# Kernel tuning notes

Measured on AMD Instinct MI355X. Metric: run time of the kernel, lower is better.

## Reference

```python
import jax, jax.numpy as jnp
import numpy as np

S = 128           # seq_len
B = 256           # input_bits (bits per token, also neurons per head)
H = 16            # num_heads
NB = 12           # n_bits_per_neuron -> LUT size 2^12
PB = 7            # relative-position bits = ceil(log2(max_seq_len))
HEAD_IN = 2 * B + PB   # concat(query, key, rel_pos_bits) = 519
THRESH = H // 2


def setup_inputs() -> dict:
    key = jax.random.key(0)
    k1, k2, k3 = jax.random.split(key, 3)
    tokens = jax.random.randint(k1, (S, B), 0, 2, dtype=jnp.int32)           # binary token bits
    memory = jax.random.normal(k2, (H, B, 2 ** NB), dtype=jnp.float32)       # RAM LUT contents per head/neuron
    connections = jax.random.randint(k3, (H, B, NB), 0, HEAD_IN, dtype=jnp.int32)  # per-neuron input-bit wiring
    return {"tokens": tokens, "memory": memory, "connections": connections}


def reference(tokens, memory, connections):
    idx = jnp.arange(S)
    rel = idx[:, None] - idx[None, :]                         # [S,S] i - j
    mask = (rel >= 0).astype(jnp.int32)                        # causal mask (j <= i)
    relc = jnp.clip(rel, 0, S - 1)
    # relative-distance binary encoding, LSB first: [S,S,PB]
    pos_bits = ((relc[..., None] >> jnp.arange(PB)) & 1).astype(jnp.int32)
    q = jnp.broadcast_to(tokens[:, None, :], (S, S, B))
    k = jnp.broadcast_to(tokens[None, :, :], (S, S, B))
    head_in = jnp.concatenate([q, k, pos_bits], axis=-1)       # [S,S,HEAD_IN]
    # RAM address per (query i, key j, head h, neuron n): pack NB wired bits, LSB first
    addr = jnp.zeros((S, S, H, B), dtype=jnp.int32)
    for b in range(NB):  # tiny fixed loop over bit planes, fully vectorized over S,S,H,B
        addr = addr + (head_in[..., connections[:, :, b]] << b)
    # LUT gather: memory[h, n, addr] -> [S,S,H,B]
    h_idx = jnp.arange(H)[:, None]
    n_idx = jnp.arange(B)[None, :]
    vals = memory[h_idx, n_idx, addr]
    bits = (vals > 0.0).astype(jnp.int32)                      # RAM neuron output bit
    # XOR accumulation over attended keys == masked sum mod 2: [S,H,B]
    head_res = jnp.sum(bits * mask[:, :, None, None], axis=1) % 2
    # majority vote across heads per bit
    ones_count = jnp.sum(head_res, axis=1)                     # [S,B]
    return (ones_count > THRESH).astype(jnp.int32)
```

## Files before the change

kernel.cpp:

```cpp
#include <hip/hip_runtime.h>
#include <hip/hip_bf16.h>


#define S 128
#define B 256
#define H 16
#define NB 12

__device__ __forceinline__ unsigned sig(unsigned x) {
    return x ^ ((x >> 3) & 0x70u) ^ ((x >> 6) & 0x70u);
}

__global__ __launch_bounds__(1024) void softram_kernel(
    const int* __restrict__ tokens,
    const float* __restrict__ memory,
    const int* __restrict__ connections,
    int* __restrict__ out)
{
    const int n    = blockIdx.x;
    const int tid  = threadIdx.x;
    const int h    = tid >> 6;
    const int lane = tid & 63;

    __shared__ unsigned char  bytetab[H * 4096];
    __shared__ unsigned int   tokT[8][S];
    __shared__ unsigned short aqsig[H][S];
    __shared__ unsigned short aksig[H][S];
    __shared__ unsigned short apsig[H][S];
    __shared__ int            conns[H][NB];
    __shared__ unsigned int   parts[H][4];

    {
        int i = tid >> 3, w = tid & 7;
        const int4* tp = (const int4*)tokens;
        unsigned v = 0;
        #pragma unroll
        for (int u = 0; u < 8; ++u) {
            int4 x = tp[i * 64 + w * 8 + u];
            v |= (unsigned)(x.x & 1) << (4 * u + 0);
            v |= (unsigned)(x.y & 1) << (4 * u + 1);
            v |= (unsigned)(x.z & 1) << (4 * u + 2);
            v |= (unsigned)(x.w & 1) << (4 * u + 3);
        }
        tokT[w][i] = v;
    }
    if (tid < H * NB) {
        int hh = tid / NB, b = tid - hh * NB;
        conns[hh][b] = connections[hh * (B * NB) + n * NB + b];
    }
    __syncthreads();

    const float4* mrow = (const float4*)(memory + ((size_t)(h * 256 + n) << 12));
    float4 va[16];
    #pragma unroll
    for (int t = 0; t < 16; ++t) va[t] = mrow[lane + 64 * t];

    unsigned qmask = 0, kmask = 0, pmask = 0;
    #pragma unroll
    for (int b = 0; b < NB; ++b) {
        int c = conns[h][b];
        qmask |= (unsigned)(c < 256) << b;
        kmask |= (unsigned)(c >= 256 && c < 512) << b;
        pmask |= (unsigned)(c >= 512) << b;
    }

    #pragma unroll
    for (int e = 0; e < 2; ++e) {
        int ii = lane + 64 * e;
        unsigned aq = 0, ak = 0, ap = 0;
        #pragma unroll
        for (int b = 0; b < NB; ++b) {
            int c = conns[h][b];
            if (c < 256) {
                aq |= ((tokT[c >> 5][ii] >> (c & 31)) & 1u) << b;
            } else if (c < 512) {
                int c2 = c - 256;
                ak |= ((tokT[c2 >> 5][ii] >> (c2 & 31)) & 1u) << b;
            } else {
                ap |= ((unsigned)(ii >> (c - 512)) & 1u) << b;
            }
        }
        aqsig[h][ii] = (unsigned short)sig(aq);
        aksig[h][ii] = (unsigned short)sig(ak);
        apsig[h][ii] = (unsigned short)sig(ap);
    }

    unsigned char* __restrict__ bt = &bytetab[h << 12];
    #pragma unroll
    for (int t = 0; t < 16; ++t) {
        float4 v = va[t];
        unsigned p = 4u * (unsigned)(lane + 64 * t);
        unsigned w = (unsigned)(v.x > 0.f)
                   | ((unsigned)(v.y > 0.f) << 8)
                   | ((unsigned)(v.z > 0.f) << 16)
                   | ((unsigned)(v.w > 0.f) << 24);
        *(unsigned*)&bt[sig(p)] = w;
    }

    unsigned long long rlo = 0, rhi = 0;

    if (pmask == 0) {
        int qb = __popc(qmask), kb = __popc(kmask);
        bool sideQ = (qb <= kb);
        unsigned smask = sideQ ? qmask : kmask;
        int m = sideQ ? qb : kb;
        unsigned spread = 0;
        {
            unsigned k = (unsigned)lane;
            #pragma unroll
            for (int b = 0; b < NB; ++b) {
                if ((smask >> b) & 1u) { spread |= (k & 1u) << b; k >>= 1; }
            }
        }
        const unsigned spv = sig(spread);
        const int lim = 1 << m;
        const bool lv = (lane < lim);
        const unsigned long long vmask =
            (lim >= 64) ? ~0ull : ((1ull << lim) - 1ull);

        if (sideQ) {
            unsigned acc = 0;
            for (int s8 = 0; s8 < 16; ++s8) {
                uint4 uq = *(const uint4*)&aqsig[h][s8 * 8];
                uint4 uk = *(const uint4*)&aksig[h][s8 * 8];
                #pragma unroll
                for (int t = 0; t < 8; ++t) {
                    int j = s8 * 8 + t;
                    unsigned cwk = ((const unsigned*)&uk)[t >> 1];
                    unsigned cwq = ((const unsigned*)&uq)[t >> 1];
                    unsigned akv = (cwk >> ((t & 1) * 16)) & 0xffffu;
                    unsigned aqv = (cwq >> ((t & 1) * 16)) & 0xffffu;
                    acc ^= bt[akv ^ spv];
                    unsigned long long accB = __ballot((acc & 1u) != 0u);
                    unsigned long long mm   = __ballot(lv && (spv == aqv));
                    unsigned long long bit  = ((accB & mm & vmask) != 0ull);
                    if (j < 64) rlo |= bit << j; else rhi |= bit << (j - 64);
                }
            }
        } else {
            unsigned c = 0;
            for (int s8 = 0; s8 < 16; ++s8) {
                uint4 uq = *(const uint4*)&aqsig[h][s8 * 8];
                uint4 uk = *(const uint4*)&aksig[h][s8 * 8];
                #pragma unroll
                for (int t = 0; t < 8; ++t) {
                    int i = s8 * 8 + t;
                    unsigned cwk = ((const unsigned*)&uk)[t >> 1];
                    unsigned cwq = ((const unsigned*)&uq)[t >> 1];
                    unsigned akv = (cwk >> ((t & 1) * 16)) & 0xffffu;
                    unsigned aqv = (cwq >> ((t & 1) * 16)) & 0xffffu;
                    c ^= (unsigned)(lv && (spv == akv));
                    unsigned sb = bt[aqv ^ spv];
                    unsigned long long mb = __ballot((c & sb & 1u) != 0u);
                    unsigned long long bit = (unsigned long long)
                        (__popcll(mb & vmask) & 1ull);
                    if (i < 64) rlo |= bit << i; else rhi |= bit << (i - 64);
                }
            }
        }
    } else {
        const unsigned ak0 = aksig[h][lane];
        const unsigned ak1 = aksig[h][lane + 64];
        for (int s8 = 0; s8 < 16; ++s8) {
            uint4 uq = *(const uint4*)&aqsig[h][s8 * 8];
            #pragma unroll
            for (int t = 0; t < 8; ++t) {
                int i = s8 * 8 + t;
                unsigned cwq = ((const unsigned*)&uq)[t >> 1];
                unsigned aqv = (cwq >> ((t & 1) * 16)) & 0xffffu;
                unsigned ap0 = apsig[h][(i - lane) & 127];
                unsigned v0  = bt[aqv ^ ak0 ^ ap0];
                unsigned long long m0 = __ballot((v0 & 1u) != 0u);
                unsigned long long pre0 =
                    (i >= 63) ? ~0ull : ((2ull << i) - 1ull);
                unsigned cnt = (unsigned)__popcll(m0 & pre0);
                if (i >= 64) {
                    unsigned ap1 = apsig[h][(i - lane - 64) & 127];
                    unsigned v1  = bt[aqv ^ ak1 ^ ap1];
                    unsigned long long m1 = __ballot((v1 & 1u) != 0u);
                    unsigned long long pre1 =
                        (i >= 127) ? ~0ull : ((2ull << (i - 64)) - 1ull);
                    cnt += (unsigned)__popcll(m1 & pre1);
                }
                unsigned long long bit = cnt & 1u;
                if (i < 64) rlo |= bit << i; else rhi |= bit << (i - 64);
            }
        }
    }

    if (lane == 0) {
        parts[h][0] = (unsigned)rlo;
        parts[h][1] = (unsigned)(rlo >> 32);
        parts[h][2] = (unsigned)rhi;
        parts[h][3] = (unsigned)(rhi >> 32);
    }
    __syncthreads();

    if (tid < S) {
        int i = tid, tot = 0;
        #pragma unroll
        for (int hh = 0; hh < H; ++hh)
            tot += (parts[hh][i >> 5] >> (i & 31)) & 1;
        out[i * B + n] = (tot > (H / 2)) ? 1 : 0;
    }
}

extern "C" void kernel_launch(void* const* d_in, const int* in_sizes, int n_in,
                              void* d_out, int out_size, void* d_ws, size_t ws_size,
                              hipStream_t stream) {
    const int*   tokens      = (const int*)d_in[0];
    const float* memory      = (const float*)d_in[1];
    const int*   connections = (const int*)d_in[2];
    int*         out         = (int*)d_out;
    (void)in_sizes; (void)n_in; (void)out_size; (void)d_ws; (void)ws_size;

    softram_kernel<<<B, 1024, 0, stream>>>(tokens, memory, connections, out);
}
```

Baseline: 112.3 us.

## Restructure no-position path into lane-indexed LUT bitmask with scalar key prefix XOR

```diff
diff --git a/kernel.cpp b/kernel.cpp
--- a/kernel.cpp
+++ b/kernel.cpp
@@ -1,5 +1,4 @@
 #include <hip/hip_runtime.h>
-#include <hip/hip_bf16.h>
 
 
 #define S 128
@@ -11,7 +10,7 @@
     return x ^ ((x >> 3) & 0x70u) ^ ((x >> 6) & 0x70u);
 }
 
-__global__ __launch_bounds__(1024) void softram_kernel(
+__global__ __launch_bounds__(1024, 4) void softram_kernel(
     const int* __restrict__ tokens,
     const float* __restrict__ memory,
     const int* __restrict__ connections,
@@ -24,11 +23,15 @@
 
     __shared__ unsigned char  bytetab[H * 4096];
     __shared__ unsigned int   tokT[8][S];
-    __shared__ unsigned short aqsig[H][S];
-    __shared__ unsigned short aksig[H][S];
-    __shared__ unsigned short apsig[H][S];
+    __shared__ unsigned short akT[H][S];
+    __shared__ unsigned short apt[H][S];
     __shared__ int            conns[H][NB];
     __shared__ unsigned int   parts[H][4];
+
+    const float4* mrow = (const float4*)(memory + ((size_t)(h * 256 + n) << 12));
+    float4 va[16];
+    #pragma unroll
+    for (int t = 0; t < 16; ++t) va[t] = mrow[lane + 64 * t];
 
     {
         int i = tid >> 3, w = tid & 7;
@@ -49,11 +52,6 @@
         conns[hh][b] = connections[hh * (B * NB) + n * NB + b];
     }
     __syncthreads();
-
-    const float4* mrow = (const float4*)(memory + ((size_t)(h * 256 + n) << 12));
-    float4 va[16];
-    #pragma unroll
-    for (int t = 0; t < 16; ++t) va[t] = mrow[lane + 64 * t];
 
     unsigned qmask = 0, kmask = 0, pmask = 0;
     #pragma unroll
@@ -63,129 +61,214 @@
         kmask |= (unsigned)(c >= 256 && c < 512) << b;
         pmask |= (unsigned)(c >= 512) << b;
     }
-
-    #pragma unroll
-    for (int e = 0; e < 2; ++e) {
-        int ii = lane + 64 * e;
-        unsigned aq = 0, ak = 0, ap = 0;
-        #pragma unroll
-        for (int b = 0; b < NB; ++b) {
-            int c = conns[h][b];
-            if (c < 256) {
-                aq |= ((tokT[c >> 5][ii] >> (c & 31)) & 1u) << b;
-            } else if (c < 512) {
-                int c2 = c - 256;
-                ak |= ((tokT[c2 >> 5][ii] >> (c2 & 31)) & 1u) << b;
-            } else {
-                ap |= ((unsigned)(ii >> (c - 512)) & 1u) << b;
-            }
-        }
-        aqsig[h][ii] = (unsigned short)sig(aq);
-        aksig[h][ii] = (unsigned short)sig(ak);
-        apsig[h][ii] = (unsigned short)sig(ap);
-    }
+    const int qb = __popc(qmask);
+    const int kb = __popc(kmask);
 
     unsigned char* __restrict__ bt = &bytetab[h << 12];
-    #pragma unroll
-    for (int t = 0; t < 16; ++t) {
-        float4 v = va[t];
-        unsigned p = 4u * (unsigned)(lane + 64 * t);
-        unsigned w = (unsigned)(v.x > 0.f)
-                   | ((unsigned)(v.y > 0.f) << 8)
-                   | ((unsigned)(v.z > 0.f) << 16)
-                   | ((unsigned)(v.w > 0.f) << 24);
-        *(unsigned*)&bt[sig(p)] = w;
-    }
-
     unsigned long long rlo = 0, rhi = 0;
 
     if (pmask == 0) {
-        int qb = __popc(qmask), kb = __popc(kmask);
-        bool sideQ = (qb <= kb);
-        unsigned smask = sideQ ? qmask : kmask;
-        int m = sideQ ? qb : kb;
-        unsigned spread = 0;
+        unsigned qcls0 = 0, qcls1 = 0;
+        #pragma unroll
+        for (int e = 0; e < 2; ++e) {
+            int ii = lane + 64 * e;
+            unsigned qc = 0, kc = 0;
+            int qn = 0, kn = 0;
+            #pragma unroll
+            for (int b = 0; b < NB; ++b) {
+                int c = conns[h][b];
+                if (c < 256) {
+                    qc |= ((tokT[c >> 5][ii] >> (c & 31)) & 1u) << qn;
+                    ++qn;
+                } else {
+                    int c2 = c - 256;
+                    kc |= ((tokT[c2 >> 5][ii] >> (c2 & 31)) & 1u) << kn;
+                    ++kn;
+                }
+            }
+            akT[h][ii] = (unsigned short)kc;
+            if (e == 0) qcls0 = qc; else qcls1 = qc;
+        }
+
+        #pragma unroll
+        for (int t = 0; t < 16; ++t) {
+            float4 v = va[t];
+            unsigned p = 4u * (unsigned)(lane + 64 * t);
+            unsigned w = (unsigned)(v.x > 0.f)
+                       | ((unsigned)(v.y > 0.f) << 8)
+                       | ((unsigned)(v.z > 0.f) << 16)
+                       | ((unsigned)(v.w > 0.f) << 24);
+            *(unsigned*)&bt[sig(p)] = w;
+        }
+
+        const bool formA = (qb <= 6);
+        const int SBITS  = formA ? qb : kb;
+        unsigned apl = 0, aul = 0;
         {
-            unsigned k = (unsigned)lane;
+            int scnt = 0, lcnt = 0;
             #pragma unroll
             for (int b = 0; b < NB; ++b) {
-                if ((smask >> b) & 1u) { spread |= (k & 1u) << b; k >>= 1; }
-            }
-        }
-        const unsigned spv = sig(spread);
-        const int lim = 1 << m;
-        const bool lv = (lane < lim);
-        const unsigned long long vmask =
-            (lim >= 64) ? ~0ull : ((1ull << lim) - 1ull);
-
-        if (sideQ) {
-            unsigned acc = 0;
-            for (int s8 = 0; s8 < 16; ++s8) {
-                uint4 uq = *(const uint4*)&aqsig[h][s8 * 8];
-                uint4 uk = *(const uint4*)&aksig[h][s8 * 8];
+                int c = conns[h][b];
+                bool isS = formA ? (c < 256) : (c >= 256);
+                if (isS) {
+                    apl |= (((unsigned)lane >> scnt) & 1u) << b;
+                    ++scnt;
+                } else {
+                    int p = SBITS + lcnt;
+                    if (p < 6) apl |= (((unsigned)lane >> p) & 1u) << b;
+                    else       aul |= (((unsigned)lane >> (p - 6)) & 1u) << b;
+                    ++lcnt;
+                }
+            }
+        }
+        const unsigned spl  = sig(apl);
+        const unsigned saul = sig(aul);
+        unsigned Wlo = 0, Whi = 0;
+        #pragma unroll 8
+        for (int it = 0; it < 64; ++it) {
+            unsigned sau  = (unsigned)__builtin_amdgcn_readlane((int)saul, it);
+            unsigned bitv = bt[sau ^ spl] & 1u;
+            unsigned long long Bm = __ballot(bitv != 0u);
+            Wlo = (lane == it) ? (unsigned)Bm : Wlo;
+            Whi = (lane == it) ? (unsigned)(Bm >> 32) : Whi;
+        }
+
+        if (formA) {
+            unsigned long long A = 0, cap0 = 0, cap1 = 0;
+            for (int s8 = 0; s8 < 8; ++s8) {
+                uint4 uk = *(const uint4*)&akT[h][s8 * 8];
                 #pragma unroll
                 for (int t = 0; t < 8; ++t) {
                     int j = s8 * 8 + t;
-                    unsigned cwk = ((const unsigned*)&uk)[t >> 1];
-                    unsigned cwq = ((const unsigned*)&uq)[t >> 1];
-                    unsigned akv = (cwk >> ((t & 1) * 16)) & 0xffffu;
-                    unsigned aqv = (cwq >> ((t & 1) * 16)) & 0xffffu;
-                    acc ^= bt[akv ^ spv];
-                    unsigned long long accB = __ballot((acc & 1u) != 0u);
-                    unsigned long long mm   = __ballot(lv && (spv == aqv));
-                    unsigned long long bit  = ((accB & mm & vmask) != 0ull);
-                    if (j < 64) rlo |= bit << j; else rhi |= bit << (j - 64);
-                }
-            }
-        } else {
-            unsigned c = 0;
-            for (int s8 = 0; s8 < 16; ++s8) {
-                uint4 uq = *(const uint4*)&aqsig[h][s8 * 8];
-                uint4 uk = *(const uint4*)&aksig[h][s8 * 8];
+                    unsigned w = ((const unsigned*)&uk)[t >> 1];
+                    unsigned widx = (unsigned)__builtin_amdgcn_readfirstlane(
+                        (int)((w >> ((t & 1) * 16)) & 0xffffu));
+                    unsigned g0 = widx << qb;
+                    int lsel = (int)(g0 >> 6);
+                    unsigned lo = (unsigned)__builtin_amdgcn_readlane((int)Wlo, lsel);
+                    unsigned hi = (unsigned)__builtin_amdgcn_readlane((int)Whi, lsel);
+                    A ^= ((((unsigned long long)hi << 32) | lo) >> (g0 & 63u));
+                    cap0 = (lane == j) ? A : cap0;
+                }
+            }
+            for (int s8 = 8; s8 < 16; ++s8) {
+                uint4 uk = *(const uint4*)&akT[h][s8 * 8];
                 #pragma unroll
                 for (int t = 0; t < 8; ++t) {
-                    int i = s8 * 8 + t;
-                    unsigned cwk = ((const unsigned*)&uk)[t >> 1];
-                    unsigned cwq = ((const unsigned*)&uq)[t >> 1];
-                    unsigned akv = (cwk >> ((t & 1) * 16)) & 0xffffu;
-                    unsigned aqv = (cwq >> ((t & 1) * 16)) & 0xffffu;
-                    c ^= (unsigned)(lv && (spv == akv));
-                    unsigned sb = bt[aqv ^ spv];
-                    unsigned long long mb = __ballot((c & sb & 1u) != 0u);
-                    unsigned long long bit = (unsigned long long)
-                        (__popcll(mb & vmask) & 1ull);
-                    if (i < 64) rlo |= bit << i; else rhi |= bit << (i - 64);
-                }
-            }
+                    int j = s8 * 8 + t;
+                    unsigned w = ((const unsigned*)&uk)[t >> 1];
+                    unsigned widx = (unsigned)__builtin_amdgcn_readfirstlane(
+                        (int)((w >> ((t & 1) * 16)) & 0xffffu));
+                    unsigned g0 = widx << qb;
+                    int lsel = (int)(g0 >> 6);
+                    unsigned lo = (unsigned)__builtin_amdgcn_readlane((int)Wlo, lsel);
+                    unsigned hi = (unsigned)__builtin_amdgcn_readlane((int)Whi, lsel);
+                    A ^= ((((unsigned long long)hi << 32) | lo) >> (g0 & 63u));
+                    cap1 = (lane == j - 64) ? A : cap1;
+                }
+            }
+            rlo = __ballot(((cap0 >> qcls0) & 1ull) != 0ull);
+            rhi = __ballot(((cap1 >> qcls1) & 1ull) != 0ull);
+        } else {
+            unsigned Cw = 0, cap0 = 0, cap1 = 0;
+            for (int s8 = 0; s8 < 8; ++s8) {
+                uint4 uk = *(const uint4*)&akT[h][s8 * 8];
+                #pragma unroll
+                for (int t = 0; t < 8; ++t) {
+                    int j = s8 * 8 + t;
+                    unsigned w = ((const unsigned*)&uk)[t >> 1];
+                    unsigned widx = (unsigned)__builtin_amdgcn_readfirstlane(
+                        (int)((w >> ((t & 1) * 16)) & 0xffffu));
+                    Cw ^= 1u << widx;
+                    cap0 = (lane == j) ? Cw : cap0;
+                }
+            }
+            for (int s8 = 8; s8 < 16; ++s8) {
+                uint4 uk = *(const uint4*)&akT[h][s8 * 8];
+                #pragma unroll
+                for (int t = 0; t < 8; ++t) {
+                    int j = s8 * 8 + t;
+                    unsigned w = ((const unsigned*)&uk)[t >> 1];
+                    unsigned widx = (unsigned)__builtin_amdgcn_readfirstlane(
+                        (int)((w >> ((t & 1) * 16)) & 0xffffu));
+                    Cw ^= 1u << widx;
+                    cap1 = (lane == j - 64) ? Cw : cap1;
+                }
+            }
+            unsigned g0a = qcls0 << kb, g0b = qcls1 << kb;
+            unsigned lo0 = (unsigned)__shfl((int)Wlo, (int)(g0a >> 6));
+            unsigned hi0 = (unsigned)__shfl((int)Whi, (int)(g0a >> 6));
+            unsigned lo1 = (unsigned)__shfl((int)Wlo, (int)(g0b >> 6));
+            unsigned hi1 = (unsigned)__shfl((int)Whi, (int)(g0b >> 6));
+            unsigned W0 = (unsigned)((((unsigned long long)hi0 << 32) | lo0) >> (g0a & 63u));
+            unsigned W1 = (unsigned)((((unsigned long long)hi1 << 32) | lo1) >> (g0b & 63u));
+            rlo = __ballot((__popc(W0 & cap0) & 1) != 0);
+            rhi = __ballot((__popc(W1 & cap1) & 1) != 0);
         }
     } else {
-        const unsigned ak0 = aksig[h][lane];
-        const unsigned ak1 = aksig[h][lane + 64];
-        for (int s8 = 0; s8 < 16; ++s8) {
-            uint4 uq = *(const uint4*)&aqsig[h][s8 * 8];
+        unsigned aqv0 = 0, aqv1 = 0;
+        #pragma unroll
+        for (int e = 0; e < 2; ++e) {
+            int ii = lane + 64 * e;
+            unsigned aq = 0, ak = 0, ap = 0;
+            #pragma unroll
+            for (int b = 0; b < NB; ++b) {
+                int c = conns[h][b];
+                if (c < 256) {
+                    aq |= ((tokT[c >> 5][ii] >> (c & 31)) & 1u) << b;
+                } else if (c < 512) {
+                    int c2 = c - 256;
+                    ak |= ((tokT[c2 >> 5][ii] >> (c2 & 31)) & 1u) << b;
+                } else {
+                    ap |= (((unsigned)ii >> (c - 512)) & 1u) << b;
+                }
+            }
+            akT[h][ii] = (unsigned short)sig(ak);
+            apt[h][ii] = (unsigned short)sig(ap);
+            if (e == 0) aqv0 = sig(aq); else aqv1 = sig(aq);
+        }
+
+        #pragma unroll
+        for (int t = 0; t < 16; ++t) {
+            float4 v = va[t];
+            unsigned p = 4u * (unsigned)(lane + 64 * t);
+            unsigned w = (unsigned)(v.x > 0.f)
+                       | ((unsigned)(v.y > 0.f) << 8)
+                       | ((unsigned)(v.z > 0.f) << 16)
+                       | ((unsigned)(v.w > 0.f) << 24);
+            *(unsigned*)&bt[sig(p)] = w;
+        }
+
+        unsigned acc0 = 0, acc1 = 0;
+        for (int s8 = 0; s8 < 8; ++s8) {
+            uint4 uk = *(const uint4*)&akT[h][s8 * 8];
             #pragma unroll
             for (int t = 0; t < 8; ++t) {
-                int i = s8 * 8 + t;
-                unsigned cwq = ((const unsigned*)&uq)[t >> 1];
-                unsigned aqv = (cwq >> ((t & 1) * 16)) & 0xffffu;
-                unsigned ap0 = apsig[h][(i - lane) & 127];
-                unsigned v0  = bt[aqv ^ ak0 ^ ap0];
-                unsigned long long m0 = __ballot((v0 & 1u) != 0u);
-                unsigned long long pre0 =
-                    (i >= 63) ? ~0ull : ((2ull << i) - 1ull);
-                unsigned cnt = (unsigned)__popcll(m0 & pre0);
-                if (i >= 64) {
-                    unsigned ap1 = apsig[h][(i - lane - 64) & 127];
-                    unsigned v1  = bt[aqv ^ ak1 ^ ap1];
-                    unsigned long long m1 = __ballot((v1 & 1u) != 0u);
-                    unsigned long long pre1 =
-                        (i >= 127) ? ~0ull : ((2ull << (i - 64)) - 1ull);
-                    cnt += (unsigned)__popcll(m1 & pre1);
-                }
-                unsigned long long bit = cnt & 1u;
-                if (i < 64) rlo |= bit << i; else rhi |= bit << (i - 64);
-            }
-        }
+                int j = s8 * 8 + t;
+                unsigned w = ((const unsigned*)&uk)[t >> 1];
+                unsigned akv = (w >> ((t & 1) * 16)) & 0xffffu;
+                int d0 = lane - j;
+                unsigned v0 = bt[aqv0 ^ akv ^ (unsigned)apt[h][d0 & 127]] & 1u;
+                acc0 ^= (d0 >= 0) ? v0 : 0u;
+                int d1 = lane + 64 - j;
+                unsigned v1 = bt[aqv1 ^ akv ^ (unsigned)apt[h][d1]] & 1u;
+                acc1 ^= v1;
+            }
+        }
+        for (int s8 = 8; s8 < 16; ++s8) {
+            uint4 uk = *(const uint4*)&akT[h][s8 * 8];
+            #pragma unroll
+            for (int t = 0; t < 8; ++t) {
+                int j = s8 * 8 + t;
+                unsigned w = ((const unsigned*)&uk)[t >> 1];
+                unsigned akv = (w >> ((t & 1) * 16)) & 0xffffu;
+                int d1 = lane + 64 - j;
+                unsigned v1 = bt[aqv1 ^ akv ^ (unsigned)apt[h][d1 & 127]] & 1u;
+                acc1 ^= (d1 >= 0) ? v1 : 0u;
+            }
+        }
+        rlo = __ballot(acc0 != 0u);
+        rhi = __ballot(acc1 != 0u);
     }
 
     if (lane == 0) {
```

After: 117.0 us. +4.2%, slower.
